# Optimization experiments

Hardware: AMD Instinct MI355X
Metric: run time of the kernel (lower is better)

The kernel has to match this reference:

```python
import jax, jax.numpy as jnp
import numpy as np

H = 64  # hidden size

def _lstm_last_h(x, W_ih, W_hh, b_ih, b_hh):
    # x: [B, T]; PyTorch LSTM gate order: i, f, g, o (each H wide in 4H axis)
    B, T = x.shape
    # input_size == 1, so x @ W_ih.T == x[..., None] * W_ih[:, 0]
    xproj = x[:, :, None] * W_ih[:, 0][None, None, :] + (b_ih + b_hh)  # [B, T, 4H]
    xproj_t = jnp.swapaxes(xproj, 0, 1)  # [T, B, 4H] for scan over time

    def step(carry, xp_t):
        h, c = carry
        gates = xp_t + h @ W_hh.T  # [B, 4H]
        i = jax.nn.sigmoid(gates[:, 0 * H:1 * H])
        f = jax.nn.sigmoid(gates[:, 1 * H:2 * H])
        g = jnp.tanh(gates[:, 2 * H:3 * H])
        o = jax.nn.sigmoid(gates[:, 3 * H:4 * H])
        c = f * c + i * g
        h = o * jnp.tanh(c)
        return (h, c), None

    h0 = jnp.zeros((B, H), x.dtype)
    c0 = jnp.zeros((B, H), x.dtype)
    (h_last, _), _ = jax.lax.scan(step, (h0, c0), xproj_t)
    return h_last  # [B, H] == lstm_out[:, -1, :]


def setup_inputs() -> dict:
    key = jax.random.key(0)
    ks = jax.random.split(key, 7)
    B, T = 2048, 512
    s_ih = 1.0 / np.sqrt(H)
    return {
        "x": jax.random.normal(ks[0], (B, T), jnp.float32),
        "W_ih": jax.random.uniform(ks[1], (4 * H, 1), jnp.float32, -s_ih, s_ih),
        "W_hh": jax.random.uniform(ks[2], (4 * H, H), jnp.float32, -s_ih, s_ih),
        "b_ih": jax.random.uniform(ks[3], (4 * H,), jnp.float32, -s_ih, s_ih),
        "b_hh": jax.random.uniform(ks[4], (4 * H,), jnp.float32, -s_ih, s_ih),
        "W_d": jax.random.uniform(ks[5], (1, H), jnp.float32, -s_ih, s_ih),
        "b_d": jax.random.uniform(ks[6], (1,), jnp.float32, -s_ih, s_ih),
    }


def reference(x, W_ih, W_hh, b_ih, b_hh, W_d, b_d):
    h_last = _lstm_last_h(x, W_ih, W_hh, b_ih, b_hh)  # [B, H]
    out = h_last @ W_d.T + b_d  # [B, 1]
    return out[:, 0]  # squeeze(1) -> [B]
```

## Files before the change

kernel.cpp:

```cpp
#include <hip/hip_runtime.h>

#define TLEN 512
#define HID  64

typedef _Float16 half8 __attribute__((ext_vector_type(8)));
typedef float    f32x4 __attribute__((ext_vector_type(4)));

__device__ __forceinline__ float rcp_fast(float x) { return __builtin_amdgcn_rcpf(x); }
__device__ __forceinline__ float exp2_fast(float x) {
#if __has_builtin(__builtin_amdgcn_exp2f)
    return __builtin_amdgcn_exp2f(x);
#else
    float r; asm("v_exp_f32 %0, %1" : "=v"(r) : "v"(x)); return r;
#endif
}

__global__ __launch_bounds__(512) __attribute__((amdgpu_waves_per_eu(2, 2)))
void lstm_mfma6(const float* __restrict__ x,
                const float* __restrict__ W_ih,
                const float* __restrict__ W_hh,
                const float* __restrict__ b_ih,
                const float* __restrict__ b_hh,
                const float* __restrict__ W_d,
                const float* __restrict__ b_d,
                float* __restrict__ out) {
    __shared__ __align__(16) float    xs[8][516];
    __shared__ __align__(16) _Float16 hbuf[2][8][72];

    const int tid = threadIdx.x;
    const int L   = tid & 63;
    const int w   = tid >> 6;
    const int r0  = blockIdx.x * 8;

    for (int i = tid; i < 8 * 128; i += 512) {
        const int r = i >> 7, t4 = (i & 127) * 4;
        *(float4*)&xs[r][t4] = *(const float4*)&x[(size_t)(r0 + r) * TLEN + t4];
    }
    for (int i = tid; i < 2 * 8 * 72; i += 512)
        ((_Float16*)hbuf)[i] = (_Float16)0.0f;

    half8 af[2][2];
    {
        const int m = L & 15;
        const int g = m & 3;
        const int kb = (L >> 4) * 8;
#pragma unroll
        for (int tt = 0; tt < 2; ++tt) {
            const int uu = 8 * w + 4 * tt + (m >> 2);
            const float* row = &W_hh[(size_t)(g * HID + uu) * HID];
#pragma unroll
            for (int q = 0; q < 2; ++q) {
                const float* p = row + 32 * q + kb;
                half8 hf;
#pragma unroll
                for (int i = 0; i < 8; ++i) hf[i] = (_Float16)p[i];
                af[tt][q] = hf;
            }
        }
    }

    const int c   = L & 15;
    const int b   = c & 7;
    const int dup = (c >> 3) & 1;
    const int u   = 8 * w + 4 * dup + (L >> 4);

    const float K = 1.44269504f;
    float wih[4], bias[4], dscl[4];
#pragma unroll
    for (int g = 0; g < 4; ++g) {
        const float s = (g == 2) ? 2.0f * K : -K;
        wih[g]  = s * W_ih[g * HID + u];
        bias[g] = s * (b_ih[g * HID + u] + b_hh[g * HID + u]);
        dscl[g] = s;
    }

    const float* xrow = &xs[b][0];
    const int koff = (L >> 4) * 8;
    const _Float16* h0r = &hbuf[0][b][0];
    _Float16*       h0w = &hbuf[0][0][0];
    const _Float16* h1r = &hbuf[1][b][0];
    _Float16*       h1w = &hbuf[1][0][0];
    const int widx = b * 72 + u;
    const f32x4 zero = {0.0f, 0.0f, 0.0f, 0.0f};
    float cst = 0.0f;

    __syncthreads();

    auto step = [&](const _Float16* hin, _Float16* hout, float xt) {
        half8 b0 = *(const half8*)(hin + koff);
        half8 b1 = *(const half8*)(hin + koff + 32);

        f32x4 d0 = __builtin_amdgcn_mfma_f32_16x16x32_f16(af[0][0], b0, zero, 0, 0, 0);
        f32x4 d1 = __builtin_amdgcn_mfma_f32_16x16x32_f16(af[1][0], b0, zero, 0, 0, 0);
        d0 = __builtin_amdgcn_mfma_f32_16x16x32_f16(af[0][1], b1, d0, 0, 0, 0);
        d1 = __builtin_amdgcn_mfma_f32_16x16x32_f16(af[1][1], b1, d1, 0, 0, 0);

        const f32x4 d = dup ? d1 : d0;

        const float ei = exp2_fast(fmaf(d[0], dscl[0], fmaf(xt, wih[0], bias[0])));
        const float ef = exp2_fast(fmaf(d[1], dscl[1], fmaf(xt, wih[1], bias[1])));
        const float eg = exp2_fast(fmaf(d[2], dscl[2], fmaf(xt, wih[2], bias[2])));
        const float eo = exp2_fast(fmaf(d[3], dscl[3], fmaf(xt, wih[3], bias[3])));
        const float gi = rcp_fast(1.0f + ei);
        const float gf = rcp_fast(1.0f + ef);
        const float gg = fmaf(-2.0f, rcp_fast(1.0f + eg), 1.0f);
        const float go = rcp_fast(1.0f + eo);
        cst = fmaf(gf, cst, gi * gg);
        const float tc = fmaf(-2.0f, rcp_fast(1.0f + exp2_fast(2.0f * K * cst)), 1.0f);
        hout[widx] = (_Float16)(go * tc);
    };

    for (int t = 0; t < TLEN; t += 2) {
        step(h0r, h1w, xrow[t]);
        __syncthreads();
        step(h1r, h0w, xrow[t + 1]);
        __syncthreads();
    }

    float pv = (float)hbuf[0][w][L] * W_d[L];
#pragma unroll
    for (int off = 32; off > 0; off >>= 1)
        pv += __shfl_xor(pv, off, 64);
    if (L == 0)
        out[r0 + w] = pv + b_d[0];
}

extern "C" void kernel_launch(void* const* d_in, const int* in_sizes, int n_in,
                              void* d_out, int out_size, void* d_ws, size_t ws_size,
                              hipStream_t stream) {
    const float* x    = (const float*)d_in[0];
    const float* W_ih = (const float*)d_in[1];
    const float* W_hh = (const float*)d_in[2];
    const float* b_ih = (const float*)d_in[3];
    const float* b_hh = (const float*)d_in[4];
    const float* W_d  = (const float*)d_in[5];
    const float* b_d  = (const float*)d_in[6];
    float* out = (float*)d_out;

    dim3 grid(256);
    dim3 block(512);
    lstm_mfma6<<<grid, block, 0, stream>>>(x, W_ih, W_hh, b_ih, b_hh, W_d, b_d, out);
}
```

Measured before the change: 221.3 us.

## Halve block to 4 waves, each computing 16 hidden units for two batch groups

Each block now uses 4 waves instead of 8. Each wave owns 16 hidden units and processes two independent groups of 4 batch rows, A and B, with separate h buffers and cell states. This issues 16 MFMAs per step instead of 4 and halves the number of waves taking part in each per-timestep barrier. In exchange there is more serial work per wave, more registers for 8 A-fragments, and lower wave occupancy. Each MFMA now covers only 4 useful batch columns out of 16.

Measured after the change: 336.9 us. 52.2% more time.

```diff
diff --git a/kernel.cpp b/kernel.cpp
--- a/kernel.cpp
+++ b/kernel.cpp
@@ -15,8 +15,8 @@
 #endif
 }
 
-__global__ __launch_bounds__(512) __attribute__((amdgpu_waves_per_eu(2, 2)))
-void lstm_mfma6(const float* __restrict__ x,
+__global__ __launch_bounds__(256) __attribute__((amdgpu_waves_per_eu(1, 1)))
+void lstm_mfma7(const float* __restrict__ x,
                 const float* __restrict__ W_ih,
                 const float* __restrict__ W_hh,
                 const float* __restrict__ b_ih,
@@ -25,28 +25,31 @@
                 const float* __restrict__ b_d,
                 float* __restrict__ out) {
     __shared__ __align__(16) float    xs[8][516];
-    __shared__ __align__(16) _Float16 hbuf[2][8][72];
+    __shared__ __align__(16) _Float16 ha[2][4][72];
+    __shared__ __align__(16) _Float16 hb[2][4][72];
 
     const int tid = threadIdx.x;
     const int L   = tid & 63;
     const int w   = tid >> 6;
     const int r0  = blockIdx.x * 8;
 
-    for (int i = tid; i < 8 * 128; i += 512) {
+    for (int i = tid; i < 8 * 128; i += 256) {
         const int r = i >> 7, t4 = (i & 127) * 4;
         *(float4*)&xs[r][t4] = *(const float4*)&x[(size_t)(r0 + r) * TLEN + t4];
     }
-    for (int i = tid; i < 2 * 8 * 72; i += 512)
-        ((_Float16*)hbuf)[i] = (_Float16)0.0f;
+    for (int i = tid; i < 2 * 4 * 72; i += 256) {
+        ((_Float16*)ha)[i] = (_Float16)0.0f;
+        ((_Float16*)hb)[i] = (_Float16)0.0f;
+    }
 
-    half8 af[2][2];
+    half8 af[4][2];
     {
         const int m = L & 15;
         const int g = m & 3;
         const int kb = (L >> 4) * 8;
 #pragma unroll
-        for (int tt = 0; tt < 2; ++tt) {
-            const int uu = 8 * w + 4 * tt + (m >> 2);
+        for (int tt = 0; tt < 4; ++tt) {
+            const int uu = 16 * w + 4 * tt + (m >> 2);
             const float* row = &W_hh[(size_t)(g * HID + uu) * HID];
 #pragma unroll
             for (int q = 0; q < 2; ++q) {
@@ -60,9 +63,9 @@
     }
 
     const int c   = L & 15;
-    const int b   = c & 7;
-    const int dup = (c >> 3) & 1;
-    const int u   = 8 * w + 4 * dup + (L >> 4);
+    const int b4  = c & 3;
+    const int sel = (c >> 2) & 3;
+    const int u   = 16 * w + 4 * sel + (L >> 4);
 
     const float K = 1.44269504f;
     float wih[4], bias[4], dscl[4];
@@ -74,29 +77,15 @@
         dscl[g] = s;
     }
 
-    const float* xrow = &xs[b][0];
+    const float* xrA = &xs[b4][0];
+    const float* xrB = &xs[b4 + 4][0];
     const int koff = (L >> 4) * 8;
-    const _Float16* h0r = &hbuf[0][b][0];
-    _Float16*       h0w = &hbuf[0][0][0];
-    const _Float16* h1r = &hbuf[1][b][0];
-    _Float16*       h1w = &hbuf[1][0][0];
-    const int widx = b * 72 + u;
     const f32x4 zero = {0.0f, 0.0f, 0.0f, 0.0f};
-    float cst = 0.0f;
+    float cA = 0.0f, cB = 0.0f;
 
     __syncthreads();
 
-    auto step = [&](const _Float16* hin, _Float16* hout, float xt) {
-        half8 b0 = *(const half8*)(hin + koff);
-        half8 b1 = *(const half8*)(hin + koff + 32);
-
-        f32x4 d0 = __builtin_amdgcn_mfma_f32_16x16x32_f16(af[0][0], b0, zero, 0, 0, 0);
-        f32x4 d1 = __builtin_amdgcn_mfma_f32_16x16x32_f16(af[1][0], b0, zero, 0, 0, 0);
-        d0 = __builtin_amdgcn_mfma_f32_16x16x32_f16(af[0][1], b1, d0, 0, 0, 0);
-        d1 = __builtin_amdgcn_mfma_f32_16x16x32_f16(af[1][1], b1, d1, 0, 0, 0);
-
-        const f32x4 d = dup ? d1 : d0;
-
+    auto act = [&](const f32x4& d, float xt, float& cst) -> _Float16 {
         const float ei = exp2_fast(fmaf(d[0], dscl[0], fmaf(xt, wih[0], bias[0])));
         const float ef = exp2_fast(fmaf(d[1], dscl[1], fmaf(xt, wih[1], bias[1])));
         const float eg = exp2_fast(fmaf(d[2], dscl[2], fmaf(xt, wih[2], bias[2])));
@@ -107,22 +96,60 @@
         const float go = rcp_fast(1.0f + eo);
         cst = fmaf(gf, cst, gi * gg);
         const float tc = fmaf(-2.0f, rcp_fast(1.0f + exp2_fast(2.0f * K * cst)), 1.0f);
-        hout[widx] = (_Float16)(go * tc);
+        return (_Float16)(go * tc);
+    };
+
+    auto step = [&](int p, float xtA, float xtB) {
+        const _Float16* hA = &ha[p][b4][koff];
+        const _Float16* hB = &hb[p][b4][koff];
+        half8 a0 = *(const half8*)hA;
+        half8 a1 = *(const half8*)(hA + 32);
+        half8 g0 = *(const half8*)hB;
+        half8 g1 = *(const half8*)(hB + 32);
+
+        f32x4 dA0 = __builtin_amdgcn_mfma_f32_16x16x32_f16(af[0][0], a0, zero, 0, 0, 0);
+        f32x4 dA1 = __builtin_amdgcn_mfma_f32_16x16x32_f16(af[1][0], a0, zero, 0, 0, 0);
+        f32x4 dA2 = __builtin_amdgcn_mfma_f32_16x16x32_f16(af[2][0], a0, zero, 0, 0, 0);
+        f32x4 dA3 = __builtin_amdgcn_mfma_f32_16x16x32_f16(af[3][0], a0, zero, 0, 0, 0);
+        f32x4 dB0 = __builtin_amdgcn_mfma_f32_16x16x32_f16(af[0][0], g0, zero, 0, 0, 0);
+        f32x4 dB1 = __builtin_amdgcn_mfma_f32_16x16x32_f16(af[1][0], g0, zero, 0, 0, 0);
+        f32x4 dB2 = __builtin_amdgcn_mfma_f32_16x16x32_f16(af[2][0], g0, zero, 0, 0, 0);
+        f32x4 dB3 = __builtin_amdgcn_mfma_f32_16x16x32_f16(af[3][0], g0, zero, 0, 0, 0);
+        dA0 = __builtin_amdgcn_mfma_f32_16x16x32_f16(af[0][1], a1, dA0, 0, 0, 0);
+        dA1 = __builtin_amdgcn_mfma_f32_16x16x32_f16(af[1][1], a1, dA1, 0, 0, 0);
+        dA2 = __builtin_amdgcn_mfma_f32_16x16x32_f16(af[2][1], a1, dA2, 0, 0, 0);
+        dA3 = __builtin_amdgcn_mfma_f32_16x16x32_f16(af[3][1], a1, dA3, 0, 0, 0);
+        dB0 = __builtin_amdgcn_mfma_f32_16x16x32_f16(af[0][1], g1, dB0, 0, 0, 0);
+        dB1 = __builtin_amdgcn_mfma_f32_16x16x32_f16(af[1][1], g1, dB1, 0, 0, 0);
+        dB2 = __builtin_amdgcn_mfma_f32_16x16x32_f16(af[2][1], g1, dB2, 0, 0, 0);
+        dB3 = __builtin_amdgcn_mfma_f32_16x16x32_f16(af[3][1], g1, dB3, 0, 0, 0);
+
+        const f32x4 dA = sel == 0 ? dA0 : (sel == 1 ? dA1 : (sel == 2 ? dA2 : dA3));
+        const f32x4 dB = sel == 0 ? dB0 : (sel == 1 ? dB1 : (sel == 2 ? dB2 : dB3));
+
+        const _Float16 hvA = act(dA, xtA, cA);
+        const _Float16 hvB = act(dB, xtB, cB);
+        ha[p ^ 1][b4][u] = hvA;
+        hb[p ^ 1][b4][u] = hvB;
+        __syncthreads();
     };
 
     for (int t = 0; t < TLEN; t += 2) {
-        step(h0r, h1w, xrow[t]);
-        __syncthreads();
-        step(h1r, h0w, xrow[t + 1]);
-        __syncthreads();
+        step(0, xrA[t],     xrB[t]);
+        step(1, xrA[t + 1], xrB[t + 1]);
     }
 
-    float pv = (float)hbuf[0][w][L] * W_d[L];
+    float pv = (float)ha[0][w][L] * W_d[L];
 #pragma unroll
     for (int off = 32; off > 0; off >>= 1)
         pv += __shfl_xor(pv, off, 64);
-    if (L == 0)
-        out[r0 + w] = pv + b_d[0];
+    if (L == 0) out[r0 + w] = pv + b_d[0];
+
+    float pw = (float)hb[0][w][L] * W_d[L];
+#pragma unroll
+    for (int off = 32; off > 0; off >>= 1)
+        pw += __shfl_xor(pw, off, 64);
+    if (L == 0) out[r0 + 4 + w] = pw + b_d[0];
 }
 
 extern "C" void kernel_launch(void* const* d_in, const int* in_sizes, int n_in,
@@ -138,6 +165,6 @@
     float* out = (float*)d_out;
 
     dim3 grid(256);
-    dim3 block(512);
-    lstm_mfma6<<<grid, block, 0, stream>>>(x, W_ih, W_hh, b_ih, b_hh, W_d, b_d, out);
+    dim3 block(256);
+    lstm_mfma7<<<grid, block, 0, stream>>>(x, W_ih, W_hh, b_ih, b_hh, W_d, b_d, out);
 }
```
